# Kernel optimization log

Measured on AMD Instinct MI355X. Metric: run time of the kernel, lower is better.

Reference implementation:

```python
import jax, jax.numpy as jnp
import numpy as np
import math

B, S, E, HEAD = 4, 2048, 1024, 64  # num_heads=16 -> head_size = 1024//16


def setup_inputs() -> dict:
    key = jax.random.key(0)
    kx, kp, kq, kk, kv = jax.random.split(key, 5)
    std = math.sqrt(2.0 / (E + HEAD))
    return {
        "x": jax.random.normal(kx, (B, S, E), dtype=jnp.float32),
        "padding_mask": jax.random.randint(kp, (B, S), 0, 2, dtype=jnp.int32),
        "Wq": jax.random.normal(kq, (HEAD, E), dtype=jnp.float32) * std,
        "Wk": jax.random.normal(kk, (HEAD, E), dtype=jnp.float32) * std,
        "Wv": jax.random.normal(kv, (HEAD, E), dtype=jnp.float32) * std,
    }


def reference(x, padding_mask, Wq, Wk, Wv):
    # q,k,v: [B,S,head] via Linear (x @ W.T, no bias)
    q = jnp.einsum("bse,he->bsh", x, Wq)
    k = jnp.einsum("bse,he->bsh", x, Wk)
    v = jnp.einsum("bse,he->bsh", x, Wv)
    scores = jnp.einsum("bqh,bkh->bqk", q, k)  # [B,S,S]
    seq = x.shape[1]
    causal = jnp.tril(jnp.ones((seq, seq), dtype=jnp.float32))  # [S,S]
    mask = causal[None, :, :] * padding_mask.astype(jnp.float32)[:, None, :]  # [B,S,S]
    scores = jnp.where(mask == 0, jnp.float32(-1e9), scores)
    head_size = k.shape[-1]
    attn = jax.nn.softmax(scores / jnp.sqrt(jnp.float32(head_size)), axis=-1)
    return jnp.einsum("bqk,bkh->bqh", attn, v)
```

## Files before the change

### kernel.cpp

```cpp
#include <hip/hip_runtime.h>
#include <hip/hip_bf16.h>
#include <math.h>

#define B_ 4
#define S_ 2048
#define E_ 1024
#define H_ 64
#define NQT 32
#define SPLITS 8
#define TPS 4
#define SENT (-1.25e8f)

typedef short bf16x8 __attribute__((ext_vector_type(8)));
typedef float f32x4 __attribute__((ext_vector_type(4)));
typedef unsigned short U16;
typedef U16 u16x8 __attribute__((ext_vector_type(8)));
typedef U16 u16x4 __attribute__((ext_vector_type(4)));

__device__ __forceinline__ U16 f2bf(float f){
    unsigned u = __builtin_bit_cast(unsigned, f);
    u += 0x7fffu + ((u >> 16) & 1u);
    return (U16)(u >> 16);
}
__device__ __forceinline__ float bf2f(U16 h){
    return __builtin_bit_cast(float, ((unsigned)h) << 16);
}
#define MFMA16(a,b,c) __builtin_amdgcn_mfma_f32_16x16x32_bf16((a),(b),(c),0,0,0)

typedef const __attribute__((address_space(1))) void GvPtr;
typedef __attribute__((address_space(3))) void LdsPtr;
__device__ __forceinline__ void gload_lds16(const void* g, void* l){
    __builtin_amdgcn_global_load_lds((GvPtr*)g, (LdsPtr*)l, 16, 0, 0);
}

__global__ __launch_bounds__(256) void prep_w(
    const float* __restrict__ Wq, const float* __restrict__ Wk,
    const float* __restrict__ Wv, U16* __restrict__ Whi, U16* __restrict__ Wlo)
{
    int i4 = (blockIdx.x*256 + threadIdx.x) * 4;
    int c = i4 >> 16, rem = i4 & 65535;
    const float* src = (c==0) ? Wq : (c==1) ? Wk : Wv;
    float4 v = *(const float4*)(src + rem);
    float a[4] = {v.x, v.y, v.z, v.w};
    u16x4 hv, lv;
    #pragma unroll
    for (int j=0;j<4;j++){ U16 h = f2bf(a[j]); hv[j]=h; lv[j]=f2bf(a[j]-bf2f(h)); }
    *(u16x4*)(Whi + i4) = hv;
    *(u16x4*)(Wlo + i4) = lv;
}

__global__ __launch_bounds__(256) void qkv_kernel(
    const float* __restrict__ x, const U16* __restrict__ Whi_g,
    const U16* __restrict__ Wlo_g,
    U16* __restrict__ Qhi, U16* __restrict__ Qlo,
    U16* __restrict__ Khi, U16* __restrict__ Klo, U16* __restrict__ Vt)
{
    __shared__ __align__(16) U16 Ah[2][32*64], Al[2][32*64];
    const int m0 = blockIdx.x * 32;
    const int tid = threadIdx.x, lane = tid & 63, wv = tid >> 6;
    const int l15 = lane & 15, quad = lane >> 4;
    const int arow = tid >> 3, ag = tid & 7;

    f32x4 acc[3][2];
    #pragma unroll
    for (int c=0;c<3;c++)
    #pragma unroll
    for (int mt=0;mt<2;mt++) acc[c][mt] = f32x4{0.f,0.f,0.f,0.f};

    {
        const float* xs = x + (size_t)(m0 + arow)*E_ + ag*8;
        float4 xa = ((const float4*)xs)[0], xb = ((const float4*)xs)[1];
        float vv[8] = {xa.x,xa.y,xa.z,xa.w,xb.x,xb.y,xb.z,xb.w};
        u16x8 hv, lv;
        #pragma unroll
        for (int j=0;j<8;j++){ U16 h = f2bf(vv[j]); hv[j]=h; lv[j]=f2bf(vv[j]-bf2f(h)); }
        ((u16x8*)Ah[0])[arow*8 + ag] = hv;
        ((u16x8*)Al[0])[arow*8 + ag] = lv;
    }
    __syncthreads();

    int p = 0;
    for (int k0 = 0; k0 < E_; k0 += 64) {
        float4 xa, xb;
        const bool have = (k0 + 64 < E_);
        if (have) {
            const float* xs = x + (size_t)(m0 + arow)*E_ + k0 + 64 + ag*8;
            xa = ((const float4*)xs)[0]; xb = ((const float4*)xs)[1];
        }
        bf16x8 bh[3][2], bl[3][2];
        #pragma unroll
        for (int c=0;c<3;c++)
        #pragma unroll
        for (int kk=0;kk<2;kk++){
            const size_t wo = (size_t)c*65536 + (size_t)(wv*16 + l15)*E_ + k0 + kk*32 + quad*8;
            bh[c][kk] = *(const bf16x8*)(Whi_g + wo);
            bl[c][kk] = *(const bf16x8*)(Wlo_g + wo);
        }
        #pragma unroll
        for (int kk=0;kk<2;kk++){
            #pragma unroll
            for (int mt=0;mt<2;mt++){
                const int ai = (mt*16 + l15)*8 + kk*4 + quad;
                bf16x8 ah = ((const bf16x8*)Ah[p])[ai];
                bf16x8 al = ((const bf16x8*)Al[p])[ai];
                #pragma unroll
                for (int c=0;c<3;c++){
                    acc[c][mt] = MFMA16(ah, bh[c][kk], acc[c][mt]);
                    acc[c][mt] = MFMA16(ah, bl[c][kk], acc[c][mt]);
                    acc[c][mt] = MFMA16(al, bh[c][kk], acc[c][mt]);
                }
            }
        }
        if (have) {
            float vv[8] = {xa.x,xa.y,xa.z,xa.w,xb.x,xb.y,xb.z,xb.w};
            u16x8 hv, lv;
            #pragma unroll
            for (int j=0;j<8;j++){ U16 h = f2bf(vv[j]); hv[j]=h; lv[j]=f2bf(vv[j]-bf2f(h)); }
            ((u16x8*)Ah[p^1])[arow*8 + ag] = hv;
            ((u16x8*)Al[p^1])[arow*8 + ag] = lv;
        }
        __syncthreads();
        p ^= 1;
    }

    const int h = wv*16 + l15;
    #pragma unroll
    for (int mt=0;mt<2;mt++){
        const int row = m0 + mt*16 + quad*4;
        #pragma unroll
        for (int r=0;r<4;r++){
            float vq = acc[0][mt][r]; U16 hq = f2bf(vq);
            Qhi[(size_t)(row+r)*H_ + h] = hq;
            Qlo[(size_t)(row+r)*H_ + h] = f2bf(vq - bf2f(hq));
            float vk = acc[1][mt][r]; U16 hk = f2bf(vk);
            Khi[(size_t)(row+r)*H_ + h] = hk;
            Klo[(size_t)(row+r)*H_ + h] = f2bf(vk - bf2f(hk));
        }
        const int b = row >> 11, s0 = row & (S_-1);
        u16x4 pk;
        #pragma unroll
        for (int r=0;r<4;r++) pk[r] = f2bf(acc[2][mt][r]);
        *(u16x4*)(Vt + ((size_t)b*H_ + h)*S_ + s0) = pk;
    }
}

__global__ __launch_bounds__(256) void attn_kernel(
    const U16* __restrict__ Qhi, const U16* __restrict__ Qlo,
    const U16* __restrict__ Khi, const U16* __restrict__ Klo,
    const U16* __restrict__ Vt, const int* __restrict__ pad,
    float* __restrict__ Opart, float* __restrict__ mpart, float* __restrict__ lpart)
{
    const int qt = blockIdx.x, b = blockIdx.y, sp = blockIdx.z;
    const int t0 = sp * TPS;
    if (t0 > qt) return;
    const int t1 = min(t0 + TPS, qt + 1);

    __shared__ __align__(16) U16 KtH[64*64], KtL[64*64], Vts[64*64];
    __shared__ __align__(16) U16 Ps[4][16*80];

    const int tid = threadIdx.x, lane = tid & 63, wv = tid >> 6;
    const int l15 = lane & 15, quad = lane >> 4;

    const size_t qrow = (size_t)b*S_ + qt*64 + wv*16 + l15;
    bf16x8 aqh0 = *(const bf16x8*)(Qhi + qrow*H_ + quad*8);
    bf16x8 aqh1 = *(const bf16x8*)(Qhi + qrow*H_ + 32 + quad*8);
    bf16x8 aql0 = *(const bf16x8*)(Qlo + qrow*H_ + quad*8);
    bf16x8 aql1 = *(const bf16x8*)(Qlo + qrow*H_ + 32 + quad*8);

    float m_i = -INFINITY, l_i = 0.f;
    f32x4 o[4];
    #pragma unroll
    for (int i=0;i<4;i++) o[i] = f32x4{0.f,0.f,0.f,0.f};
    const int qg = qt*64 + wv*16 + l15;
    U16* Pw = &Ps[wv][0];

    for (int t = t0; t < t1; ++t) {
        const int kb = t * 64;
        __syncthreads();
        {
            const U16* kh = Khi + ((size_t)b*S_ + kb)*H_;
            const U16* kl = Klo + ((size_t)b*S_ + kb)*H_;
            #pragma unroll
            for (int ch=0; ch<2; ++ch){
                const int sb = wv*128 + ch*64;
                const int slot = sb + lane;
                gload_lds16(kh + (size_t)slot*8, (U16*)KtH + sb*8);
                gload_lds16(kl + (size_t)slot*8, (U16*)KtL + sb*8);
                const int vrow = slot >> 3, vg = slot & 7;
                gload_lds16(Vt + ((size_t)b*H_ + vrow)*S_ + kb + vg*8, (U16*)Vts + sb*8);
            }
        }
        const unsigned long long pm = __ballot(pad[(size_t)b*S_ + kb + lane] != 0);
        __syncthreads();

        f32x4 z[4];
        #pragma unroll
        for (int nt=0; nt<4; nt++){
            const int kr = (nt*16 + l15)*8;
            bf16x8 kh0 = ((const bf16x8*)KtH)[kr + quad];
            bf16x8 kh1 = ((const bf16x8*)KtH)[kr + 4 + quad];
            bf16x8 kl0 = ((const bf16x8*)KtL)[kr + quad];
            bf16x8 kl1 = ((const bf16x8*)KtL)[kr + 4 + quad];
            f32x4 zz = f32x4{0.f,0.f,0.f,0.f};
            zz = MFMA16(kh0, aqh0, zz);
            zz = MFMA16(kh1, aqh1, zz);
            zz = MFMA16(kh0, aql0, zz);
            zz = MFMA16(kh1, aql1, zz);
            zz = MFMA16(kl0, aqh0, zz);
            zz = MFMA16(kl1, aqh1, zz);
            z[nt] = zz;
        }
        float rmax = -INFINITY;
        #pragma unroll
        for (int nt=0; nt<4; nt++){
            const int rel = qg - kb - nt*16 - quad*4;
            const unsigned mb = (unsigned)(pm >> (nt*16 + quad*4)) & 0xFu;
            #pragma unroll
            for (int r=0;r<4;r++){
                const bool ok = (r <= rel) && ((mb >> r) & 1u);
                const float v = ok ? z[nt][r]*0.125f : SENT;
                z[nt][r] = v;
                rmax = fmaxf(rmax, v);
            }
        }
        rmax = fmaxf(rmax, __shfl_xor(rmax, 16));
        rmax = fmaxf(rmax, __shfl_xor(rmax, 32));
        const float mn = fmaxf(m_i, rmax);
        const float alpha = __expf(m_i - mn);
        m_i = mn;
        float rsum = 0.f;
        #pragma unroll
        for (int nt=0; nt<4; nt++)
        #pragma unroll
        for (int r=0;r<4;r++){
            const float pv = __expf(z[nt][r] - mn);
            z[nt][r] = pv;
            rsum += pv;
        }
        rsum += __shfl_xor(rsum, 16);
        rsum += __shfl_xor(rsum, 32);
        l_i = l_i*alpha + rsum;
        #pragma unroll
        for (int nt=0; nt<4; nt++)
        #pragma unroll
        for (int r=0;r<4;r++) o[nt][r] *= alpha;

        #pragma unroll
        for (int nt=0; nt<4; nt++){
            u16x4 pk;
            #pragma unroll
            for (int r=0;r<4;r++) pk[r] = f2bf(z[nt][r]);
            *(u16x4*)(Pw + l15*80 + nt*16 + quad*4) = pk;
        }
        #pragma unroll
        for (int ks=0; ks<2; ks++){
            bf16x8 bp = *(const bf16x8*)(Pw + l15*80 + ks*32 + quad*8);
            #pragma unroll
            for (int nt=0; nt<4; nt++){
                bf16x8 av = ((const bf16x8*)Vts)[(nt*16 + l15)*8 + ks*4 + quad];
                o[nt] = MFMA16(av, bp, o[nt]);
            }
        }
    }
    const size_t rbase = ((size_t)((b*NQT + qt)*SPLITS + sp))*64 + wv*16 + l15;
    if (quad == 0) { mpart[rbase] = m_i; lpart[rbase] = l_i; }
    #pragma unroll
    for (int nt=0; nt<4; nt++)
        *((f32x4*)(Opart + rbase*H_ + nt*16 + quad*4)) = o[nt];
}

__global__ __launch_bounds__(256) void combine_kernel(
    const float* __restrict__ Opart, const float* __restrict__ mpart,
    const float* __restrict__ lpart, const U16* __restrict__ Vt,
    float* __restrict__ out)
{
    const int idx = blockIdx.x*256 + threadIdx.x;
    const int h = idx & 63;
    const int q = (idx >> 6) & (S_-1);
    const int b = idx >> 17;
    const int qt = q >> 6, r = q & 63;
    const int ns = (qt >> 2) + 1;
    const size_t rb = ((size_t)(b*NQT + qt)*SPLITS)*64 + r;
    float M = -INFINITY;
    for (int s2=0; s2<ns; s2++) M = fmaxf(M, mpart[rb + (size_t)s2*64]);
    float res;
    if (M == SENT) {
        const U16* vsrc = Vt + ((size_t)b*H_ + h)*S_;
        float sm = 0.f;
        for (int s=0; s<S_; ++s) sm += bf2f(vsrc[s]);
        res = sm * (1.f/(float)S_);
    } else {
        float L = 0.f, accv = 0.f;
        for (int s2=0; s2<ns; s2++){
            const float mi = mpart[rb + (size_t)s2*64];
            const float w = __expf(mi - M);
            L    += w * lpart[rb + (size_t)s2*64];
            accv += w * Opart[(rb + (size_t)s2*64)*H_ + h];
        }
        res = accv / L;
    }
    out[idx] = res;
}

extern "C" void kernel_launch(void* const* d_in, const int* in_sizes, int n_in,
                              void* d_out, int out_size, void* d_ws, size_t ws_size,
                              hipStream_t stream)
{
    (void)in_sizes; (void)n_in; (void)out_size; (void)ws_size;
    const float* x  = (const float*)d_in[0];
    const int* pad  = (const int*)d_in[1];
    const float* Wq = (const float*)d_in[2];
    const float* Wk = (const float*)d_in[3];
    const float* Wv = (const float*)d_in[4];
    float* out = (float*)d_out;
    char* ws = (char*)d_ws;
    const size_t MB = 1u << 20;
    U16* Whi = (U16*)(ws);
    U16* Wlo = (U16*)(ws + 393216);
    U16* Qhi = (U16*)(ws + 1*MB);
    U16* Qlo = (U16*)(ws + 2*MB);
    U16* Khi = (U16*)(ws + 3*MB);
    U16* Klo = (U16*)(ws + 4*MB);
    U16* Vt  = (U16*)(ws + 5*MB);
    float* Opart = (float*)(ws + 6*MB);
    float* mpart = (float*)(ws + 22*MB);
    float* lpart = (float*)(ws + 22*MB + (1u<<18));

    prep_w<<<dim3(192), 256, 0, stream>>>(Wq, Wk, Wv, Whi, Wlo);
    qkv_kernel<<<dim3(256), 256, 0, stream>>>(x, Whi, Wlo, Qhi, Qlo, Khi, Klo, Vt);
    attn_kernel<<<dim3(NQT, B_, SPLITS), 256, 0, stream>>>(Qhi, Qlo, Khi, Klo, Vt, pad,
                                                           Opart, mpart, lpart);
    combine_kernel<<<dim3((B_*S_*H_)/256), 256, 0, stream>>>(Opart, mpart, lpart, Vt, out);
}
```

Baseline: 164.4 us.

## Fuse QKV, attention and combine into one persistent kernel with grid barriers

Replaces the separate QKV projection, split-K attention and combine kernels with a single 256-block persistent kernel. Software grid barriers built on atomics separate the phases. The QKV phase now splits K across waves and reduces through LDS. Attention uses 128-row query tiles with an XOR-swizzled LDS layout, and the fully-masked fallback precomputes V means instead of looping over S per element. The combine phase is vectorised. This removes launch overhead and the slow masked-row path, but depends on all blocks being co-resident for the spin barriers and leaves some phases underutilising the GPU.

```diff
diff --git a/kernel.cpp b/kernel.cpp
--- a/kernel.cpp
+++ b/kernel.cpp
@@ -6,10 +6,9 @@
 #define S_ 2048
 #define E_ 1024
 #define H_ 64
-#define NQT 32
-#define SPLITS 8
 #define TPS 4
 #define SENT (-1.25e8f)
+#define NBLK 256
 
 typedef short bf16x8 __attribute__((ext_vector_type(8)));
 typedef float f32x4 __attribute__((ext_vector_type(4)));
@@ -31,6 +30,18 @@
 typedef __attribute__((address_space(3))) void LdsPtr;
 __device__ __forceinline__ void gload_lds16(const void* g, void* l){
     __builtin_amdgcn_global_load_lds((GvPtr*)g, (LdsPtr*)l, 16, 0, 0);
+}
+
+__device__ __forceinline__ void grid_barrier(unsigned* cnt){
+    __syncthreads();
+    if (threadIdx.x == 0){
+        __threadfence();
+        atomicAdd(cnt, 1u);
+        while (__hip_atomic_load(cnt, __ATOMIC_ACQUIRE, __HIP_MEMORY_SCOPE_AGENT) < NBLK)
+            __builtin_amdgcn_s_sleep(2);
+        __threadfence();
+    }
+    __syncthreads();
 }
 
 __global__ __launch_bounds__(256) void prep_w(
@@ -49,257 +60,262 @@
     *(u16x4*)(Wlo + i4) = lv;
 }
 
-__global__ __launch_bounds__(256) void qkv_kernel(
-    const float* __restrict__ x, const U16* __restrict__ Whi_g,
-    const U16* __restrict__ Wlo_g,
+__global__ __launch_bounds__(512, 2) void fused_kernel(
+    const float* __restrict__ x, const int* __restrict__ pad,
+    const U16* __restrict__ Whi_g, const U16* __restrict__ Wlo_g,
     U16* __restrict__ Qhi, U16* __restrict__ Qlo,
-    U16* __restrict__ Khi, U16* __restrict__ Klo, U16* __restrict__ Vt)
+    U16* __restrict__ Khi, U16* __restrict__ Klo, U16* __restrict__ Vt,
+    float* __restrict__ Opart, float* __restrict__ mpart, float* __restrict__ lpart,
+    float* __restrict__ meanV, unsigned* __restrict__ cnt,
+    float* __restrict__ out)
 {
-    __shared__ __align__(16) U16 Ah[2][32*64], Al[2][32*64];
-    const int m0 = blockIdx.x * 32;
+    __shared__ __align__(16) char smem[73728];
     const int tid = threadIdx.x, lane = tid & 63, wv = tid >> 6;
     const int l15 = lane & 15, quad = lane >> 4;
-    const int arow = tid >> 3, ag = tid & 7;
-
-    f32x4 acc[3][2];
-    #pragma unroll
-    for (int c=0;c<3;c++)
-    #pragma unroll
-    for (int mt=0;mt<2;mt++) acc[c][mt] = f32x4{0.f,0.f,0.f,0.f};
 
     {
-        const float* xs = x + (size_t)(m0 + arow)*E_ + ag*8;
-        float4 xa = ((const float4*)xs)[0], xb = ((const float4*)xs)[1];
-        float vv[8] = {xa.x,xa.y,xa.z,xa.w,xb.x,xb.y,xb.z,xb.w};
-        u16x8 hv, lv;
+        float* Red = (float*)smem;
+        const int m0 = blockIdx.x * 32;
+        const int bb = m0 >> 11;
+        const int kq = wv & 3, mh = wv >> 2;
+
+        f32x4 acc[12];
         #pragma unroll
-        for (int j=0;j<8;j++){ U16 h = f2bf(vv[j]); hv[j]=h; lv[j]=f2bf(vv[j]-bf2f(h)); }
-        ((u16x8*)Ah[0])[arow*8 + ag] = hv;
-        ((u16x8*)Al[0])[arow*8 + ag] = lv;
+        for (int i=0;i<12;i++) acc[i] = f32x4{0.f,0.f,0.f,0.f};
+
+        const float* xb = x + (size_t)(m0 + mh*16 + l15)*E_ + kq*256 + quad*8;
+        const size_t wbase = (size_t)l15*E_ + kq*256 + quad*8;
+
+        float4 xc0 = ((const float4*)xb)[0], xc1 = ((const float4*)xb)[1];
+        #pragma unroll 1
+        for (int s=0; s<8; ++s){
+            bf16x8 ah, al;
+            {
+                float v[8] = {xc0.x,xc0.y,xc0.z,xc0.w,xc1.x,xc1.y,xc1.z,xc1.w};
+                #pragma unroll
+                for (int j2=0;j2<8;j2++){
+                    U16 h = f2bf(v[j2]);
+                    ah[j2] = (short)h;
+                    al[j2] = (short)f2bf(v[j2] - bf2f(h));
+                }
+            }
+            if (s < 7){
+                const float* xs = xb + (s+1)*32;
+                xc0 = ((const float4*)xs)[0];
+                xc1 = ((const float4*)xs)[1];
+            }
+            #pragma unroll
+            for (int c=0;c<3;++c)
+            #pragma unroll
+            for (int nt=0;nt<4;++nt){
+                const size_t o2 = (size_t)c*65536 + wbase + (size_t)nt*16*E_ + s*32;
+                bf16x8 bh = *(const bf16x8*)(Whi_g + o2);
+                bf16x8 bl = *(const bf16x8*)(Wlo_g + o2);
+                acc[c*4+nt] = MFMA16(ah, bh, acc[c*4+nt]);
+                acc[c*4+nt] = MFMA16(ah, bl, acc[c*4+nt]);
+                acc[c*4+nt] = MFMA16(al, bh, acc[c*4+nt]);
+            }
+        }
+        if (kq != 0){
+            float* rp = Red + (size_t)((kq-1)*2 + mh)*12*64*4;
+            #pragma unroll
+            for (int a=0;a<12;++a) *(f32x4*)(rp + (a*64 + lane)*4) = acc[a];
+        }
+        __syncthreads();
+        if (kq == 0){
+            #pragma unroll
+            for (int k2=0;k2<3;++k2){
+                const float* rp = Red + (size_t)(k2*2 + mh)*12*64*4;
+                #pragma unroll
+                for (int a=0;a<12;++a) acc[a] += *(const f32x4*)(rp + (a*64 + lane)*4);
+            }
+            #pragma unroll
+            for (int nt=0;nt<4;++nt){
+                const int h = nt*16 + l15;
+                const int row = m0 + mh*16 + quad*4;
+                #pragma unroll
+                for (int r=0;r<4;++r){
+                    float vq = acc[nt][r];   U16 hq = f2bf(vq);
+                    Qhi[(size_t)(row+r)*H_ + h] = hq;
+                    Qlo[(size_t)(row+r)*H_ + h] = f2bf(vq - bf2f(hq));
+                    float vk = acc[4+nt][r]; U16 hk = f2bf(vk);
+                    Khi[(size_t)(row+r)*H_ + h] = hk;
+                    Klo[(size_t)(row+r)*H_ + h] = f2bf(vk - bf2f(hk));
+                }
+                u16x4 pk;
+                #pragma unroll
+                for (int r=0;r<4;++r) pk[r] = f2bf(acc[8+nt][r]);
+                *(u16x4*)(Vt + ((size_t)bb*H_ + h)*S_ + (row & (S_-1))) = pk;
+            }
+        }
     }
-    __syncthreads();
-
-    int p = 0;
-    for (int k0 = 0; k0 < E_; k0 += 64) {
-        float4 xa, xb;
-        const bool have = (k0 + 64 < E_);
-        if (have) {
-            const float* xs = x + (size_t)(m0 + arow)*E_ + k0 + 64 + ag*8;
-            xa = ((const float4*)xs)[0]; xb = ((const float4*)xs)[1];
-        }
-        bf16x8 bh[3][2], bl[3][2];
-        #pragma unroll
-        for (int c=0;c<3;c++)
-        #pragma unroll
-        for (int kk=0;kk<2;kk++){
-            const size_t wo = (size_t)c*65536 + (size_t)(wv*16 + l15)*E_ + k0 + kk*32 + quad*8;
-            bh[c][kk] = *(const bf16x8*)(Whi_g + wo);
-            bl[c][kk] = *(const bf16x8*)(Wlo_g + wo);
-        }
-        #pragma unroll
-        for (int kk=0;kk<2;kk++){
-            #pragma unroll
-            for (int mt=0;mt<2;mt++){
-                const int ai = (mt*16 + l15)*8 + kk*4 + quad;
-                bf16x8 ah = ((const bf16x8*)Ah[p])[ai];
-                bf16x8 al = ((const bf16x8*)Al[p])[ai];
-                #pragma unroll
-                for (int c=0;c<3;c++){
-                    acc[c][mt] = MFMA16(ah, bh[c][kk], acc[c][mt]);
-                    acc[c][mt] = MFMA16(ah, bl[c][kk], acc[c][mt]);
-                    acc[c][mt] = MFMA16(al, bh[c][kk], acc[c][mt]);
+    grid_barrier(cnt + 0);
+
+    {
+        U16* KtH = (U16*)smem;
+        U16* KtL = KtH + 4096;
+        U16* Vts = KtL + 4096;
+        U16* Ps  = Vts + 4096;
+
+        if (blockIdx.x >= 224){
+            const int idx = (blockIdx.x - 224)*8 + wv;
+            const U16* vp = Vt + (size_t)idx*S_;
+            float sm = 0.f;
+            #pragma unroll
+            for (int it2=0; it2<4; ++it2){
+                u16x8 d = *(const u16x8*)(vp + (it2*64 + lane)*8);
+                #pragma unroll
+                for (int j2=0;j2<8;j2++) sm += bf2f(d[j2]);
+            }
+            #pragma unroll
+            for (int m2=1; m2<=32; m2<<=1) sm += __shfl_xor(sm, m2);
+            if (lane == 0) meanV[idx] = sm;
+        }
+
+        const int srow = tid >> 3, sg = tid & 7, sgs = sg ^ (srow & 7);
+        const int sb16 = wv*512;
+        const int sw = l15 & 7;
+
+        for (int rd=0; rd<2; ++rd){
+            const int n = blockIdx.x + rd*NBLK;
+            if (n >= 288) continue;
+            const int b = n & 3;
+            int j = n >> 2, q = 15;
+            for (;;){ const int c = (q>>1)+1; if (j < c) break; j -= c; --q; }
+            const int sp = j;
+            const int t0 = sp*TPS, t1 = min(t0+TPS, 2*q+2);
+
+            const size_t qrow = (size_t)b*S_ + q*128 + wv*16 + l15;
+            bf16x8 aqh0 = *(const bf16x8*)(Qhi + qrow*H_ + quad*8);
+            bf16x8 aqh1 = *(const bf16x8*)(Qhi + qrow*H_ + 32 + quad*8);
+            bf16x8 aql0 = *(const bf16x8*)(Qlo + qrow*H_ + quad*8);
+            bf16x8 aql1 = *(const bf16x8*)(Qlo + qrow*H_ + 32 + quad*8);
+
+            float m_i = -INFINITY, l_i = 0.f;
+            f32x4 o[4];
+            #pragma unroll
+            for (int i=0;i<4;i++) o[i] = f32x4{0.f,0.f,0.f,0.f};
+            const int qg = q*128 + wv*16 + l15;
+            const int qmax = q*128 + wv*16 + 15;
+            U16* Pw = Ps + wv*1280;
+
+            for (int t=t0; t<t1; ++t){
+                const int kb = t*64;
+                __syncthreads();
+                gload_lds16(Khi + ((size_t)b*S_ + kb + srow)*H_ + sgs*8, KtH + sb16);
+                gload_lds16(Klo + ((size_t)b*S_ + kb + srow)*H_ + sgs*8, KtL + sb16);
+                gload_lds16(Vt + ((size_t)b*H_ + srow)*S_ + kb + sgs*8, Vts + sb16);
+                const unsigned long long pm = __ballot(pad[(size_t)b*S_ + kb + lane] != 0);
+                __syncthreads();
+
+                if (kb <= qmax){
+                    f32x4 z[4];
+                    #pragma unroll
+                    for (int nt=0; nt<4; nt++){
+                        const int kr = (nt*16 + l15)*8;
+                        bf16x8 kh0 = ((const bf16x8*)KtH)[kr + (quad ^ sw)];
+                        bf16x8 kh1 = ((const bf16x8*)KtH)[kr + ((4+quad) ^ sw)];
+                        bf16x8 kl0 = ((const bf16x8*)KtL)[kr + (quad ^ sw)];
+                        bf16x8 kl1 = ((const bf16x8*)KtL)[kr + ((4+quad) ^ sw)];
+                        f32x4 zz = f32x4{0.f,0.f,0.f,0.f};
+                        zz = MFMA16(kh0, aqh0, zz);
+                        zz = MFMA16(kh1, aqh1, zz);
+                        zz = MFMA16(kh0, aql0, zz);
+                        zz = MFMA16(kh1, aql1, zz);
+                        zz = MFMA16(kl0, aqh0, zz);
+                        zz = MFMA16(kl1, aqh1, zz);
+                        z[nt] = zz;
+                    }
+                    float rmax = -INFINITY;
+                    #pragma unroll
+                    for (int nt=0; nt<4; nt++){
+                        const int rel = qg - kb - nt*16 - quad*4;
+                        const unsigned mb = (unsigned)(pm >> (nt*16 + quad*4)) & 0xFu;
+                        #pragma unroll
+                        for (int r=0;r<4;r++){
+                            const bool ok = (r <= rel) && ((mb >> r) & 1u);
+                            const float v = ok ? z[nt][r]*0.125f : SENT;
+                            z[nt][r] = v;
+                            rmax = fmaxf(rmax, v);
+                        }
+                    }
+                    rmax = fmaxf(rmax, __shfl_xor(rmax, 16));
+                    rmax = fmaxf(rmax, __shfl_xor(rmax, 32));
+                    const float mn = fmaxf(m_i, rmax);
+                    const float alpha = __expf(m_i - mn);
+                    m_i = mn;
+                    float rsum = 0.f;
+                    #pragma unroll
+                    for (int nt=0; nt<4; nt++)
+                    #pragma unroll
+                    for (int r=0;r<4;r++){
+                        const float pe = __expf(z[nt][r] - mn);
+                        z[nt][r] = pe;
+                        rsum += pe;
+                    }
+                    rsum += __shfl_xor(rsum, 16);
+                    rsum += __shfl_xor(rsum, 32);
+                    l_i = l_i*alpha + rsum;
+                    #pragma unroll
+                    for (int nt=0; nt<4; nt++)
+                    #pragma unroll
+                    for (int r=0;r<4;r++) o[nt][r] *= alpha;
+
+                    #pragma unroll
+                    for (int nt=0; nt<4; nt++){
+                        u16x4 pk;
+                        #pragma unroll
+                        for (int r=0;r<4;r++) pk[r] = f2bf(z[nt][r]);
+                        *(u16x4*)(Pw + l15*80 + nt*16 + quad*4) = pk;
+                    }
+                    #pragma unroll
+                    for (int ks=0; ks<2; ks++){
+                        bf16x8 bp = *(const bf16x8*)(Pw + l15*80 + ks*32 + quad*8);
+                        #pragma unroll
+                        for (int nt=0; nt<4; nt++){
+                            bf16x8 av2 = ((const bf16x8*)Vts)[(nt*16 + l15)*8 + ((ks*4+quad) ^ sw)];
+                            o[nt] = MFMA16(av2, bp, o[nt]);
+                        }
+                    }
                 }
             }
-        }
-        if (have) {
-            float vv[8] = {xa.x,xa.y,xa.z,xa.w,xb.x,xb.y,xb.z,xb.w};
-            u16x8 hv, lv;
-            #pragma unroll
-            for (int j=0;j<8;j++){ U16 h = f2bf(vv[j]); hv[j]=h; lv[j]=f2bf(vv[j]-bf2f(h)); }
-            ((u16x8*)Ah[p^1])[arow*8 + ag] = hv;
-            ((u16x8*)Al[p^1])[arow*8 + ag] = lv;
-        }
-        __syncthreads();
-        p ^= 1;
+            const size_t rbase = ((size_t)((b*16 + q)*8 + sp))*128 + wv*16 + l15;
+            if (quad == 0){ mpart[rbase] = m_i; lpart[rbase] = l_i; }
+            #pragma unroll
+            for (int nt=0; nt<4; nt++)
+                *(f32x4*)(Opart + rbase*64 + nt*16 + quad*4) = o[nt];
+        }
     }
-
-    const int h = wv*16 + l15;
-    #pragma unroll
-    for (int mt=0;mt<2;mt++){
-        const int row = m0 + mt*16 + quad*4;
-        #pragma unroll
-        for (int r=0;r<4;r++){
-            float vq = acc[0][mt][r]; U16 hq = f2bf(vq);
-            Qhi[(size_t)(row+r)*H_ + h] = hq;
-            Qlo[(size_t)(row+r)*H_ + h] = f2bf(vq - bf2f(hq));
-            float vk = acc[1][mt][r]; U16 hk = f2bf(vk);
-            Khi[(size_t)(row+r)*H_ + h] = hk;
-            Klo[(size_t)(row+r)*H_ + h] = f2bf(vk - bf2f(hk));
-        }
-        const int b = row >> 11, s0 = row & (S_-1);
-        u16x4 pk;
-        #pragma unroll
-        for (int r=0;r<4;r++) pk[r] = f2bf(acc[2][mt][r]);
-        *(u16x4*)(Vt + ((size_t)b*H_ + h)*S_ + s0) = pk;
+    grid_barrier(cnt + 1);
+
+    {
+        const int base = (blockIdx.x*512 + tid)*4;
+        const int h0 = base & 63;
+        const int qq = (base >> 6) & (S_-1);
+        const int b3 = base >> 17;
+        const int q128 = qq >> 7, r = qq & 127;
+        const int ns = (q128 >> 1) + 1;
+        const size_t rb = ((size_t)(b3*16 + q128)*8)*128 + r;
+        float M = -INFINITY;
+        for (int s2=0; s2<ns; ++s2) M = fmaxf(M, mpart[rb + (size_t)s2*128]);
+        f32x4 res;
+        if (M == SENT){
+            #pragma unroll
+            for (int j2=0;j2<4;j2++) res[j2] = meanV[b3*64 + h0 + j2] * (1.f/(float)S_);
+        } else {
+            float L = 0.f;
+            f32x4 av = f32x4{0.f,0.f,0.f,0.f};
+            for (int s2=0; s2<ns; ++s2){
+                const float mi = mpart[rb + (size_t)s2*128];
+                const float w = __expf(mi - M);
+                L += w * lpart[rb + (size_t)s2*128];
+                const f32x4 op = *(const f32x4*)(Opart + (rb + (size_t)s2*128)*64 + h0);
+                av += op * w;
+            }
+            res = av * (1.f / L);
+        }
+        *(f32x4*)(out + base) = res;
     }
-}
-
-__global__ __launch_bounds__(256) void attn_kernel(
-    const U16* __restrict__ Qhi, const U16* __restrict__ Qlo,
-    const U16* __restrict__ Khi, const U16* __restrict__ Klo,
-    const U16* __restrict__ Vt, const int* __restrict__ pad,
-    float* __restrict__ Opart, float* __restrict__ mpart, float* __restrict__ lpart)
-{
-    const int qt = blockIdx.x, b = blockIdx.y, sp = blockIdx.z;
-    const int t0 = sp * TPS;
-    if (t0 > qt) return;
-    const int t1 = min(t0 + TPS, qt + 1);
-
-    __shared__ __align__(16) U16 KtH[64*64], KtL[64*64], Vts[64*64];
-    __shared__ __align__(16) U16 Ps[4][16*80];
-
-    const int tid = threadIdx.x, lane = tid & 63, wv = tid >> 6;
-    const int l15 = lane & 15, quad = lane >> 4;
-
-    const size_t qrow = (size_t)b*S_ + qt*64 + wv*16 + l15;
-    bf16x8 aqh0 = *(const bf16x8*)(Qhi + qrow*H_ + quad*8);
-    bf16x8 aqh1 = *(const bf16x8*)(Qhi + qrow*H_ + 32 + quad*8);
-    bf16x8 aql0 = *(const bf16x8*)(Qlo + qrow*H_ + quad*8);
-    bf16x8 aql1 = *(const bf16x8*)(Qlo + qrow*H_ + 32 + quad*8);
-
-    float m_i = -INFINITY, l_i = 0.f;
-    f32x4 o[4];
-    #pragma unroll
-    for (int i=0;i<4;i++) o[i] = f32x4{0.f,0.f,0.f,0.f};
-    const int qg = qt*64 + wv*16 + l15;
-    U16* Pw = &Ps[wv][0];
-
-    for (int t = t0; t < t1; ++t) {
-        const int kb = t * 64;
-        __syncthreads();
-        {
-            const U16* kh = Khi + ((size_t)b*S_ + kb)*H_;
-            const U16* kl = Klo + ((size_t)b*S_ + kb)*H_;
-            #pragma unroll
-            for (int ch=0; ch<2; ++ch){
-                const int sb = wv*128 + ch*64;
-                const int slot = sb + lane;
-                gload_lds16(kh + (size_t)slot*8, (U16*)KtH + sb*8);
-                gload_lds16(kl + (size_t)slot*8, (U16*)KtL + sb*8);
-                const int vrow = slot >> 3, vg = slot & 7;
-                gload_lds16(Vt + ((size_t)b*H_ + vrow)*S_ + kb + vg*8, (U16*)Vts + sb*8);
-            }
-        }
-        const unsigned long long pm = __ballot(pad[(size_t)b*S_ + kb + lane] != 0);
-        __syncthreads();
-
-        f32x4 z[4];
-        #pragma unroll
-        for (int nt=0; nt<4; nt++){
-            const int kr = (nt*16 + l15)*8;
-            bf16x8 kh0 = ((const bf16x8*)KtH)[kr + quad];
-            bf16x8 kh1 = ((const bf16x8*)KtH)[kr + 4 + quad];
-            bf16x8 kl0 = ((const bf16x8*)KtL)[kr + quad];
-            bf16x8 kl1 = ((const bf16x8*)KtL)[kr + 4 + quad];
-            f32x4 zz = f32x4{0.f,0.f,0.f,0.f};
-            zz = MFMA16(kh0, aqh0, zz);
-            zz = MFMA16(kh1, aqh1, zz);
-            zz = MFMA16(kh0, aql0, zz);
-            zz = MFMA16(kh1, aql1, zz);
-            zz = MFMA16(kl0, aqh0, zz);
-            zz = MFMA16(kl1, aqh1, zz);
-            z[nt] = zz;
-        }
-        float rmax = -INFINITY;
-        #pragma unroll
-        for (int nt=0; nt<4; nt++){
-            const int rel = qg - kb - nt*16 - quad*4;
-            const unsigned mb = (unsigned)(pm >> (nt*16 + quad*4)) & 0xFu;
-            #pragma unroll
-            for (int r=0;r<4;r++){
-                const bool ok = (r <= rel) && ((mb >> r) & 1u);
-                const float v = ok ? z[nt][r]*0.125f : SENT;
-                z[nt][r] = v;
-                rmax = fmaxf(rmax, v);
-            }
-        }
-        rmax = fmaxf(rmax, __shfl_xor(rmax, 16));
-        rmax = fmaxf(rmax, __shfl_xor(rmax, 32));
-        const float mn = fmaxf(m_i, rmax);
-        const float alpha = __expf(m_i - mn);
-        m_i = mn;
-        float rsum = 0.f;
-        #pragma unroll
-        for (int nt=0; nt<4; nt++)
-        #pragma unroll
-        for (int r=0;r<4;r++){
-            const float pv = __expf(z[nt][r] - mn);
-            z[nt][r] = pv;
-            rsum += pv;
-        }
-        rsum += __shfl_xor(rsum, 16);
-        rsum += __shfl_xor(rsum, 32);
-        l_i = l_i*alpha + rsum;
-        #pragma unroll
-        for (int nt=0; nt<4; nt++)
-        #pragma unroll
-        for (int r=0;r<4;r++) o[nt][r] *= alpha;
-
-        #pragma unroll
-        for (int nt=0; nt<4; nt++){
-            u16x4 pk;
-            #pragma unroll
-            for (int r=0;r<4;r++) pk[r] = f2bf(z[nt][r]);
-            *(u16x4*)(Pw + l15*80 + nt*16 + quad*4) = pk;
-        }
-        #pragma unroll
-        for (int ks=0; ks<2; ks++){
-            bf16x8 bp = *(const bf16x8*)(Pw + l15*80 + ks*32 + quad*8);
-            #pragma unroll
-            for (int nt=0; nt<4; nt++){
-                bf16x8 av = ((const bf16x8*)Vts)[(nt*16 + l15)*8 + ks*4 + quad];
-                o[nt] = MFMA16(av, bp, o[nt]);
-            }
-        }
-    }
-    const size_t rbase = ((size_t)((b*NQT + qt)*SPLITS + sp))*64 + wv*16 + l15;
-    if (quad == 0) { mpart[rbase] = m_i; lpart[rbase] = l_i; }
-    #pragma unroll
-    for (int nt=0; nt<4; nt++)
-        *((f32x4*)(Opart + rbase*H_ + nt*16 + quad*4)) = o[nt];
-}
-
-__global__ __launch_bounds__(256) void combine_kernel(
-    const float* __restrict__ Opart, const float* __restrict__ mpart,
-    const float* __restrict__ lpart, const U16* __restrict__ Vt,
-    float* __restrict__ out)
-{
-    const int idx = blockIdx.x*256 + threadIdx.x;
-    const int h = idx & 63;
-    const int q = (idx >> 6) & (S_-1);
-    const int b = idx >> 17;
-    const int qt = q >> 6, r = q & 63;
-    const int ns = (qt >> 2) + 1;
-    const size_t rb = ((size_t)(b*NQT + qt)*SPLITS)*64 + r;
-    float M = -INFINITY;
-    for (int s2=0; s2<ns; s2++) M = fmaxf(M, mpart[rb + (size_t)s2*64]);
-    float res;
-    if (M == SENT) {
-        const U16* vsrc = Vt + ((size_t)b*H_ + h)*S_;
-        float sm = 0.f;
-        for (int s=0; s<S_; ++s) sm += bf2f(vsrc[s]);
-        res = sm * (1.f/(float)S_);
-    } else {
-        float L = 0.f, accv = 0.f;
-        for (int s2=0; s2<ns; s2++){
-            const float mi = mpart[rb + (size_t)s2*64];
-            const float w = __expf(mi - M);
-            L    += w * lpart[rb + (size_t)s2*64];
-            accv += w * Opart[(rb + (size_t)s2*64)*H_ + h];
-        }
-        res = accv / L;
-    }
-    out[idx] = res;
 }
 
 extern "C" void kernel_launch(void* const* d_in, const int* in_sizes, int n_in,
@@ -316,7 +332,7 @@
     char* ws = (char*)d_ws;
     const size_t MB = 1u << 20;
     U16* Whi = (U16*)(ws);
-    U16* Wlo = (U16*)(ws + 393216);
+    U16* Wlo = (U16*)(ws + MB/2);
     U16* Qhi = (U16*)(ws + 1*MB);
     U16* Qlo = (U16*)(ws + 2*MB);
     U16* Khi = (U16*)(ws + 3*MB);
@@ -325,10 +341,12 @@
     float* Opart = (float*)(ws + 6*MB);
     float* mpart = (float*)(ws + 22*MB);
     float* lpart = (float*)(ws + 22*MB + (1u<<18));
-
+    float* meanV = (float*)(ws + 22*MB + 2*(1u<<18));
+    unsigned* cnt = (unsigned*)(ws + 22*MB + 2*(1u<<18) + 4096);
+
+    hipMemsetAsync(cnt, 0, 64, stream);
     prep_w<<<dim3(192), 256, 0, stream>>>(Wq, Wk, Wv, Whi, Wlo);
-    qkv_kernel<<<dim3(256), 256, 0, stream>>>(x, Whi, Wlo, Qhi, Qlo, Khi, Klo, Vt);
-    attn_kernel<<<dim3(NQT, B_, SPLITS), 256, 0, stream>>>(Qhi, Qlo, Khi, Klo, Vt, pad,
-                                                           Opart, mpart, lpart);
-    combine_kernel<<<dim3((B_*S_*H_)/256), 256, 0, stream>>>(Opart, mpart, lpart, Vt, out);
-}
+    fused_kernel<<<dim3(NBLK), 512, 0, stream>>>(x, pad, Whi, Wlo,
+                                                 Qhi, Qlo, Khi, Klo, Vt,
+                                                 Opart, mpart, lpart, meanV, cnt, out);
+}
```

New measurement: 208.6 us. 26.9% more time.
